# Kernel tuning notes

Measured on AMD Instinct MI355X. Metric: run time of the kernel, lower is better.

## Reference

```python
import jax, jax.numpy as jnp
import numpy as np

NUM_LESION_CLS = 8
MAX_INST = 64          # instance ids in mask_gt are < MAX_INST
SIZE_TH = 100.0
# merge_classes=[[1],...,[8]] -> zero-based groups [0..7] => identity merge


def setup_inputs() -> dict:
    key = jax.random.key(0)
    k1, k2, k3 = jax.random.split(key, 3)
    B, H, W, K = 32, 1024, 1024, 64
    pred_class = jax.random.normal(k1, (B, NUM_LESION_CLS), dtype=jnp.float32)
    mask_gt = jax.random.randint(k2, (B, H, W), 0, MAX_INST, dtype=jnp.int32)
    label_gt = jax.random.randint(k3, (B, K, 2), 0, 32, dtype=jnp.int64)
    return {"pred_class": pred_class, "mask_gt": mask_gt, "label_gt": label_gt}


def reference(pred_class, mask_gt, label_gt):
    # Per-sample histogram of instance-id pixel counts: [B, MAX_INST]
    inst_sizes = jax.vmap(lambda m: jnp.bincount(m.reshape(-1), length=MAX_INST))(mask_gt)
    inst_ids = label_gt[..., 0]            # [B, K]
    labels = label_gt[..., 1]              # [B, K]
    sizes = jnp.take_along_axis(inst_sizes, inst_ids, axis=1).astype(jnp.float32)  # [B, K]
    valid = (labels > 0) & (labels <= NUM_LESION_CLS)                              # [B, K]
    # scatter sizes into per-class counts: cnts[b, label-1] += size (if valid)
    onehot = jax.nn.one_hot(jnp.where(valid, labels - 1, 0), NUM_LESION_CLS,
                            dtype=jnp.float32) * valid[..., None].astype(jnp.float32)
    cnts = jnp.einsum('bk,bkc->bc', sizes, onehot)                                 # [B, C]
    # merge_classes is identity here, so class_label == cnts groups
    class_label = jnp.minimum(cnts / SIZE_TH, 1.0)
    # BCEWithLogitsLoss (mean reduction), numerically stable form
    x = pred_class
    loss = jnp.mean(jnp.maximum(x, 0.0) - x * class_label + jnp.log1p(jnp.exp(-jnp.abs(x))))
    return loss
```

## Files before the change

### kernel.cpp

```cpp
#include <hip/hip_runtime.h>
#include <math.h>

#define NB 32
#define HW (1024 * 1024)
#define BINS 64
#define KLBL 64
#define NCLS 8
#define BPI 64
#define TPB 256
#define CHUNK4 4096

__global__ __launch_bounds__(TPB) void hist_kernel(const int* __restrict__ mask,
                                                   int* __restrict__ hist) {
    __shared__ int sh[4][BINS];
    const int tid = threadIdx.x;
    const int b = blockIdx.x / BPI;
    const int part = blockIdx.x % BPI;
    const int wave = tid >> 6;

    sh[tid >> 6][tid & 63] = 0;
    __syncthreads();

    const int4* __restrict__ p4 =
        (const int4*)(mask + (size_t)b * HW) + (size_t)part * CHUNK4;

    #pragma unroll
    for (int h = 0; h < 2; ++h) {
        int4 v[8];
        #pragma unroll
        for (int k = 0; k < 8; ++k)
            v[k] = p4[(h * 8 + k) * TPB + tid];
        #pragma unroll
        for (int k = 0; k < 8; ++k) {
            atomicAdd(&sh[wave][v[k].x & 63], 1);
            atomicAdd(&sh[wave][v[k].y & 63], 1);
            atomicAdd(&sh[wave][v[k].z & 63], 1);
            atomicAdd(&sh[wave][v[k].w & 63], 1);
        }
    }
    __syncthreads();

    if (tid < BINS) {
        int s = sh[0][tid] + sh[1][tid] + sh[2][tid] + sh[3][tid];
        atomicAdd(&hist[b * BINS + tid], s);
    }
}

__global__ __launch_bounds__(TPB) void finalize_kernel(const float* __restrict__ pred,
                                                       const int* __restrict__ lg,
                                                       const int* __restrict__ hist,
                                                       float* __restrict__ out) {
    __shared__ float cnts[NB * NCLS];
    __shared__ float wsum[4];
    const int tid = threadIdx.x;

    cnts[tid] = 0.0f;
    __syncthreads();

    for (int e = tid; e < NB * KLBL; e += TPB) {
        int inst  = lg[e * 2 + 0];
        int label = lg[e * 2 + 1];
        if (label > 0 && label <= NCLS) {
            float sz = (float)hist[(e >> 6) * BINS + (inst & 63)];
            atomicAdd(&cnts[(e >> 6) * NCLS + (label - 1)], sz);
        }
    }
    __syncthreads();

    float x = pred[tid];
    float t = fminf(cnts[tid] * (1.0f / 100.0f), 1.0f);
    float l = fmaxf(x, 0.0f) - x * t + log1pf(expf(-fabsf(x)));

    for (int off = 32; off > 0; off >>= 1)
        l += __shfl_down(l, off, 64);
    if ((tid & 63) == 0) wsum[tid >> 6] = l;
    __syncthreads();
    if (tid == 0)
        out[0] = (wsum[0] + wsum[1] + wsum[2] + wsum[3]) * (1.0f / (NB * NCLS));
}

extern "C" void kernel_launch(void* const* d_in, const int* in_sizes, int n_in,
                              void* d_out, int out_size, void* d_ws, size_t ws_size,
                              hipStream_t stream) {
    const float* pred = (const float*)d_in[0];
    const int*   mask = (const int*)d_in[1];
    const int*   lg   = (const int*)d_in[2];
    float* out = (float*)d_out;
    int* hist = (int*)d_ws;

    hipMemsetAsync(hist, 0, NB * BINS * sizeof(int), stream);
    hist_kernel<<<NB * BPI, TPB, 0, stream>>>(mask, hist);
    finalize_kernel<<<1, TPB, 0, stream>>>(pred, lg, hist, out);
}
```

Baseline: 203.7 us.

## Fuse finalize into histogram kernel via last-block pattern and sub-bin LDS privatization

Merges the single-block finalize kernel into the histogram kernel. A global done counter lets the last finishing block compute the BCE loss, which removes one kernel launch and the gap between launches. It also spreads each wave's LDS histogram across four sub-copies indexed by lane group, to reduce atomic contention on the same address. The costs are larger LDS use, a threadfence plus a global atomic per block, and a serial tail run by one block.

```diff
diff --git a/kernel.cpp b/kernel.cpp
--- a/kernel.cpp
+++ b/kernel.cpp
@@ -9,16 +9,25 @@
 #define BPI 64
 #define TPB 256
 #define CHUNK4 4096
+#define SUBS 4
 
-__global__ __launch_bounds__(TPB) void hist_kernel(const int* __restrict__ mask,
-                                                   int* __restrict__ hist) {
-    __shared__ int sh[4][BINS];
-    const int tid = threadIdx.x;
-    const int b = blockIdx.x / BPI;
+__global__ __launch_bounds__(TPB) void hist_fused_kernel(
+        const float* __restrict__ pred,
+        const int*   __restrict__ mask,
+        const int*   __restrict__ lg,
+        int*         __restrict__ hist,
+        int*         __restrict__ done_cnt,
+        float*       __restrict__ out) {
+    __shared__ int sh[4][BINS][SUBS];
+    const int tid  = threadIdx.x;
+    const int b    = blockIdx.x / BPI;
     const int part = blockIdx.x % BPI;
     const int wave = tid >> 6;
+    const int sub  = (tid >> 4) & (SUBS - 1);
 
-    sh[tid >> 6][tid & 63] = 0;
+    #pragma unroll
+    for (int i = 0; i < (4 * BINS * SUBS) / TPB; ++i)
+        ((int*)sh)[i * TPB + tid] = 0;
     __syncthreads();
 
     const int4* __restrict__ p4 =
@@ -32,28 +41,36 @@
             v[k] = p4[(h * 8 + k) * TPB + tid];
         #pragma unroll
         for (int k = 0; k < 8; ++k) {
-            atomicAdd(&sh[wave][v[k].x & 63], 1);
-            atomicAdd(&sh[wave][v[k].y & 63], 1);
-            atomicAdd(&sh[wave][v[k].z & 63], 1);
-            atomicAdd(&sh[wave][v[k].w & 63], 1);
+            atomicAdd(&sh[wave][v[k].x & 63][sub], 1);
+            atomicAdd(&sh[wave][v[k].y & 63][sub], 1);
+            atomicAdd(&sh[wave][v[k].z & 63][sub], 1);
+            atomicAdd(&sh[wave][v[k].w & 63][sub], 1);
         }
     }
     __syncthreads();
 
     if (tid < BINS) {
-        int s = sh[0][tid] + sh[1][tid] + sh[2][tid] + sh[3][tid];
+        int s = 0;
+        #pragma unroll
+        for (int w = 0; w < 4; ++w)
+            #pragma unroll
+            for (int q = 0; q < SUBS; ++q)
+                s += sh[w][tid][q];
         atomicAdd(&hist[b * BINS + tid], s);
     }
-}
+    __syncthreads();
 
-__global__ __launch_bounds__(TPB) void finalize_kernel(const float* __restrict__ pred,
-                                                       const int* __restrict__ lg,
-                                                       const int* __restrict__ hist,
-                                                       float* __restrict__ out) {
+    __shared__ int isLast;
+    if (tid == 0) {
+        __threadfence();
+        isLast = (atomicAdd(done_cnt, 1) == (NB * BPI) - 1);
+    }
+    __syncthreads();
+    if (!isLast) return;
+    __threadfence();
+
     __shared__ float cnts[NB * NCLS];
     __shared__ float wsum[4];
-    const int tid = threadIdx.x;
-
     cnts[tid] = 0.0f;
     __syncthreads();
 
@@ -61,8 +78,9 @@
         int inst  = lg[e * 2 + 0];
         int label = lg[e * 2 + 1];
         if (label > 0 && label <= NCLS) {
-            float sz = (float)hist[(e >> 6) * BINS + (inst & 63)];
-            atomicAdd(&cnts[(e >> 6) * NCLS + (label - 1)], sz);
+            int szi = __hip_atomic_load(&hist[(e >> 6) * BINS + (inst & 63)],
+                                        __ATOMIC_RELAXED, __HIP_MEMORY_SCOPE_AGENT);
+            atomicAdd(&cnts[(e >> 6) * NCLS + (label - 1)], (float)szi);
         }
     }
     __syncthreads();
@@ -87,8 +105,8 @@
     const int*   lg   = (const int*)d_in[2];
     float* out = (float*)d_out;
     int* hist = (int*)d_ws;
+    int* done = hist + NB * BINS;
 
-    hipMemsetAsync(hist, 0, NB * BINS * sizeof(int), stream);
-    hist_kernel<<<NB * BPI, TPB, 0, stream>>>(mask, hist);
-    finalize_kernel<<<1, TPB, 0, stream>>>(pred, lg, hist, out);
+    hipMemsetAsync(d_ws, 0, (NB * BINS + 1) * sizeof(int), stream);
+    hist_fused_kernel<<<NB * BPI, TPB, 0, stream>>>(pred, mask, lg, hist, done, out);
 }
```

New measurement: 262.1 us. +28.7%, slower.

## Replace shared atomics with per-thread packed 16-bit private histograms

Applied to the files above, without the earlier changes.

Each thread now keeps its own 64-bin histogram in LDS, packed as two 16-bit counters per 32-bit word and laid out column-per-thread, so increments are plain read-modify-writes with no atomic contention. All 16 int4 loads are issued up front behind a scheduling barrier to increase memory-level parallelism. A strided reduction across threads then sums the packed words and flushes them to global memory. This uses 32 KB of LDS per block, which may lower occupancy, and relies on per-block counts staying below 65536 so the 16-bit fields do not overflow.

```diff
diff --git a/kernel.cpp b/kernel.cpp
--- a/kernel.cpp
+++ b/kernel.cpp
@@ -9,40 +9,56 @@
 #define BPI 64
 #define TPB 256
 #define CHUNK4 4096
+#define WORDS 32
 
 __global__ __launch_bounds__(TPB) void hist_kernel(const int* __restrict__ mask,
                                                    int* __restrict__ hist) {
-    __shared__ int sh[4][BINS];
+    __shared__ unsigned int priv[WORDS][TPB];
     const int tid = threadIdx.x;
     const int b = blockIdx.x / BPI;
     const int part = blockIdx.x % BPI;
-    const int wave = tid >> 6;
 
-    sh[tid >> 6][tid & 63] = 0;
+    {
+        uint4* z = (uint4*)&priv[0][0];
+        #pragma unroll
+        for (int i = 0; i < 8; ++i)
+            z[i * TPB + tid] = make_uint4(0u, 0u, 0u, 0u);
+    }
     __syncthreads();
 
     const int4* __restrict__ p4 =
         (const int4*)(mask + (size_t)b * HW) + (size_t)part * CHUNK4;
 
+    int4 v[16];
     #pragma unroll
-    for (int h = 0; h < 2; ++h) {
-        int4 v[8];
+    for (int k = 0; k < 16; ++k)
+        v[k] = p4[k * TPB + tid];
+    __builtin_amdgcn_sched_barrier(0);
+
+    #pragma unroll
+    for (int k = 0; k < 16; ++k) {
+        int vals[4] = {v[k].x, v[k].y, v[k].z, v[k].w};
         #pragma unroll
-        for (int k = 0; k < 8; ++k)
-            v[k] = p4[(h * 8 + k) * TPB + tid];
-        #pragma unroll
-        for (int k = 0; k < 8; ++k) {
-            atomicAdd(&sh[wave][v[k].x & 63], 1);
-            atomicAdd(&sh[wave][v[k].y & 63], 1);
-            atomicAdd(&sh[wave][v[k].z & 63], 1);
-            atomicAdd(&sh[wave][v[k].w & 63], 1);
+        for (int j = 0; j < 4; ++j) {
+            int q = vals[j] & 63;
+            priv[q >> 1][tid] += 1u << ((q & 1) << 4);
         }
     }
     __syncthreads();
 
-    if (tid < BINS) {
-        int s = sh[0][tid] + sh[1][tid] + sh[2][tid] + sh[3][tid];
-        atomicAdd(&hist[b * BINS + tid], s);
+    const int w = tid >> 3, p = tid & 7;
+    unsigned int s = 0;
+    #pragma unroll
+    for (int j = 0; j < 8; ++j) {
+        uint4 r = *(const uint4*)&priv[w][p * 32 + j * 4];
+        s += r.x + r.y + r.z + r.w;
+    }
+    #pragma unroll
+    for (int off = 4; off > 0; off >>= 1)
+        s += __shfl_down(s, off, 8);
+    if (p == 0) {
+        atomicAdd(&hist[b * BINS + 2 * w],     (int)(s & 0xFFFFu));
+        atomicAdd(&hist[b * BINS + 2 * w + 1], (int)(s >> 16));
     }
 }
 
```

Result: slower. 208.0 us (+2.1%).

## Stream mask via double-buffered global_load_lds and privatize LDS histogram sub-bins

Applied to the files above, without the earlier changes.

The histogram kernel now stages mask tiles into LDS with asynchronous global_load_lds in a two-buffer pipeline, so the next tile's load overlaps atomics on the current one. Each wave's histogram is split into four sub-copies per bin to spread LDS atomic traffic across banks and threads. Per-block partial histograms replace the memset and global atomics, and the single finalize block reduces them. The cost is more LDS use per block, half as many blocks, and a serial partial reduction in the finalize kernel.

```diff
diff --git a/kernel.cpp b/kernel.cpp
--- a/kernel.cpp
+++ b/kernel.cpp
@@ -6,53 +6,98 @@
 #define BINS 64
 #define KLBL 64
 #define NCLS 8
-#define BPI 64
 #define TPB 256
-#define CHUNK4 4096
+#define BPI 32
+#define NBLK (NB * BPI)
+#define STAGES 8
+#define STG_I4 1024
+#define WAVE_I4 256
+#define SUBS 4
 
 __global__ __launch_bounds__(TPB) void hist_kernel(const int* __restrict__ mask,
-                                                   int* __restrict__ hist) {
-    __shared__ int sh[4][BINS];
-    const int tid = threadIdx.x;
-    const int b = blockIdx.x / BPI;
-    const int part = blockIdx.x % BPI;
+                                                   int* __restrict__ part) {
+    __shared__ int4 stage[2][STG_I4];
+    __shared__ unsigned int sh[4][BINS][SUBS];
+    const int tid  = threadIdx.x;
     const int wave = tid >> 6;
+    const int lane = tid & 63;
+    const int sub  = (tid >> 4) & (SUBS - 1);
 
-    sh[tid >> 6][tid & 63] = 0;
-    __syncthreads();
+    ((uint4*)sh)[tid] = make_uint4(0u, 0u, 0u, 0u);
 
-    const int4* __restrict__ p4 =
-        (const int4*)(mask + (size_t)b * HW) + (size_t)part * CHUNK4;
+    const int b = blockIdx.x >> 5;
+    const int r = blockIdx.x & 31;
+    const int4* gbase = (const int4*)(mask + (size_t)b * HW)
+                      + (size_t)r * (STAGES * STG_I4);
 
-    #pragma unroll
-    for (int h = 0; h < 2; ++h) {
-        int4 v[8];
+    auto issue = [&](int buf, int s) {
+        const int4* gp = gbase + s * STG_I4 + wave * WAVE_I4 + lane;
+        int4* lp = &stage[buf][wave * WAVE_I4];
         #pragma unroll
-        for (int k = 0; k < 8; ++k)
-            v[k] = p4[(h * 8 + k) * TPB + tid];
+        for (int k = 0; k < 4; ++k)
+            __builtin_amdgcn_global_load_lds(
+                (const __attribute__((address_space(1))) void*)(gp + k * 64),
+                (__attribute__((address_space(3))) void*)(lp + k * 64),
+                16, 0, 0);
+    };
+
+    issue(0, 0);
+    for (int s = 0; s < STAGES; ++s) {
+        const int buf = s & 1;
+        if (s + 1 < STAGES) {
+            issue(buf ^ 1, s + 1);
+            asm volatile("s_waitcnt vmcnt(4)" ::: "memory");
+        } else {
+            asm volatile("s_waitcnt vmcnt(0)" ::: "memory");
+        }
+        __builtin_amdgcn_sched_barrier(0);
+
+        int4 v[4];
         #pragma unroll
-        for (int k = 0; k < 8; ++k) {
-            atomicAdd(&sh[wave][v[k].x & 63], 1);
-            atomicAdd(&sh[wave][v[k].y & 63], 1);
-            atomicAdd(&sh[wave][v[k].z & 63], 1);
-            atomicAdd(&sh[wave][v[k].w & 63], 1);
+        for (int j = 0; j < 4; ++j)
+            v[j] = stage[buf][wave * WAVE_I4 + j * 64 + lane];
+        #pragma unroll
+        for (int j = 0; j < 4; ++j) {
+            atomicAdd(&sh[wave][v[j].x & 63][sub], 1u);
+            atomicAdd(&sh[wave][v[j].y & 63][sub], 1u);
+            atomicAdd(&sh[wave][v[j].z & 63][sub], 1u);
+            atomicAdd(&sh[wave][v[j].w & 63][sub], 1u);
         }
     }
     __syncthreads();
 
     if (tid < BINS) {
-        int s = sh[0][tid] + sh[1][tid] + sh[2][tid] + sh[3][tid];
-        atomicAdd(&hist[b * BINS + tid], s);
+        unsigned int s = 0;
+        #pragma unroll
+        for (int w = 0; w < 4; ++w)
+            #pragma unroll
+            for (int q = 0; q < SUBS; ++q)
+                s += sh[w][tid][q];
+        part[blockIdx.x * BINS + tid] = (int)s;
     }
 }
 
 __global__ __launch_bounds__(TPB) void finalize_kernel(const float* __restrict__ pred,
                                                        const int* __restrict__ lg,
-                                                       const int* __restrict__ hist,
+                                                       const int* __restrict__ part,
                                                        float* __restrict__ out) {
+    __shared__ int hist[NB][BINS];
     __shared__ float cnts[NB * NCLS];
     __shared__ float wsum[4];
     const int tid = threadIdx.x;
+
+    const int b = tid >> 3, bg = tid & 7;
+    int4 a0 = make_int4(0, 0, 0, 0), a1 = make_int4(0, 0, 0, 0);
+    #pragma unroll 4
+    for (int blk = 0; blk < BPI; ++blk) {
+        const int* row = part + (b * BPI + blk) * BINS + bg * 8;
+        int4 r0 = *(const int4*)(row);
+        int4 r1 = *(const int4*)(row + 4);
+        a0.x += r0.x; a0.y += r0.y; a0.z += r0.z; a0.w += r0.w;
+        a1.x += r1.x; a1.y += r1.y; a1.z += r1.z; a1.w += r1.w;
+    }
+    *(int4*)&hist[b][bg * 8]     = a0;
+    *(int4*)&hist[b][bg * 8 + 4] = a1;
 
     cnts[tid] = 0.0f;
     __syncthreads();
@@ -61,7 +106,7 @@
         int inst  = lg[e * 2 + 0];
         int label = lg[e * 2 + 1];
         if (label > 0 && label <= NCLS) {
-            float sz = (float)hist[(e >> 6) * BINS + (inst & 63)];
+            float sz = (float)hist[e >> 6][inst & 63];
             atomicAdd(&cnts[(e >> 6) * NCLS + (label - 1)], sz);
         }
     }
@@ -86,9 +131,8 @@
     const int*   mask = (const int*)d_in[1];
     const int*   lg   = (const int*)d_in[2];
     float* out = (float*)d_out;
-    int* hist = (int*)d_ws;
+    int* part = (int*)d_ws;
 
-    hipMemsetAsync(hist, 0, NB * BINS * sizeof(int), stream);
-    hist_kernel<<<NB * BPI, TPB, 0, stream>>>(mask, hist);
-    finalize_kernel<<<1, TPB, 0, stream>>>(pred, lg, hist, out);
+    hist_kernel<<<NBLK, TPB, 0, stream>>>(mask, part);
+    finalize_kernel<<<1, TPB, 0, stream>>>(pred, lg, part, out);
 }
```

Result: no change. 207.3 us (+1.8%).
